# Kernel optimization log

Measured on AMD Instinct MI355X. Metric: run time of the kernel, lower is better.

The kernel has to match this reference:

```python
import jax, jax.numpy as jnp
import numpy as np

B, N, D, H = 128, 256, 256, 256
N_POWER_ITERS = 5  # matches spectral_norm(n_power_iterations=5)


def setup_inputs() -> dict:
    key = jax.random.key(0)
    ks = jax.random.split(key, 8)
    w = lambda k, shape: jax.random.normal(k, shape, dtype=jnp.float32) * 0.05
    return {
        "x": jax.random.normal(ks[0], (B, N, D), dtype=jnp.float32),
        "Wq": w(ks[1], (H, D)), "bq": w(ks[2], (H,)),
        "Wk": w(ks[3], (H, D)), "bk": w(ks[4], (H,)),
        "Wv": w(ks[5], (D, D)), "bv": w(ks[6], (D,)),
        "u0": jax.random.normal(ks[7], (D,), dtype=jnp.float32),
    }


def _l2norm(v, eps=1e-12):
    return v / (jnp.linalg.norm(v) + eps)


def _spectral_normalize(W, u0):
    # torch spectral_norm: power iteration (no grad) to get u, v; sigma = u^T W v (with grad)
    u = _l2norm(u0)
    v = _l2norm(W.T @ u)
    def body(i, uv):
        u, v = uv
        v = _l2norm(W.T @ u)
        u = _l2norm(W @ v)
        return (u, v)
    u, v = jax.lax.fori_loop(0, N_POWER_ITERS, body, (u, v))
    u = jax.lax.stop_gradient(u)
    v = jax.lax.stop_gradient(v)
    sigma = u @ (W @ v)
    return W / sigma


def reference(x, Wq, bq, Wk, bk, Wv, bv, u0):
    # torch Linear: y = x @ W.T + b, W is [out, in]
    q = jnp.einsum('bnd,hd->bnh', x, Wq) + bq          # [B, N, H]
    k = jnp.einsum('bnd,hd->bnh', x, Wk) + bk          # [B, N, H]
    Wv_sn = _spectral_normalize(Wv, u0)
    vals = jnp.einsum('bnd,od->bno', x, Wv_sn) + bv    # [B, N, D]
    scores = jnp.einsum('bnh,bmh->bnm', q, k)          # [B, N, N]
    # track_grads=False -> eigenvals detached; stop_gradient input so eig has no tangent path
    ev = jnp.linalg.eigvals(jax.lax.stop_gradient(scores))  # complex [B, N]
    rho = jnp.max(jnp.abs(ev), axis=-1)[:, None, None]      # spectral radius [B,1,1]
    attention = scores / rho
    weighted = jnp.einsum('bnm,bmd->bnd', attention, vals)  # [B, N, D]
    return weighted, attention
```

## Files before the change

kernel.cpp:

```cpp
#include <hip/hip_runtime.h>
#include <hip/hip_bf16.h>


#define NB 128
#define MAT 65536
#define BIG 8388608LL

typedef __attribute__((ext_vector_type(4))) float floatx4;
typedef __attribute__((ext_vector_type(4))) float f4v;
typedef __attribute__((ext_vector_type(8))) short short8v;
typedef __attribute__((ext_vector_type(4))) short short4v;

__device__ __forceinline__ short f2bf(float x) {
  union { float f; unsigned u; } v; v.f = x;
  unsigned r = v.u + 0x7fff + ((v.u >> 16) & 1);
  return (short)(r >> 16);
}
__device__ __forceinline__ float bf2f(short h) {
  union { unsigned u; float f; } v; v.u = ((unsigned)(unsigned short)h) << 16; return v.f;
}

template<bool TB, bool BATCHED>
__global__ __launch_bounds__(256) void gemm_mfma(
    const float* __restrict__ A, const float* __restrict__ B, float* __restrict__ C,
    long long sA, long long sB, long long sC,
    const float* __restrict__ bias,
    const float* __restrict__ scale_ptr, int sstride, int smode,
    float* __restrict__ norm_out,
    float* __restrict__ att_out,
    const float* __restrict__ B2, const float* __restrict__ bias2, float* __restrict__ C2,
    const float* __restrict__ B3, float* __restrict__ C3,
    const float* __restrict__ bsc, const float* __restrict__ bsb)
{
  __shared__ short sAhi[128 * 32], sAlo[128 * 32];
  __shared__ short sBhi[128 * 40], sBlo[128 * 40];

  int bz, m0, n0;
  if constexpr (BATCHED) {
    int lin = blockIdx.x;
    int xcd = lin & 7;
    int s = lin >> 3;
    bz = xcd * 16 + (s >> 2);
    int tile = s & 3;
    m0 = (tile >> 1) * 128;
    n0 = (tile & 1) * 128;
  } else {
    bz = 0;
    m0 = blockIdx.y * 128;
    n0 = (blockIdx.x & 1) * 128;
    int sel = blockIdx.x >> 1;
    if (sel == 1) { B = B2; bias = bias2; C = C2; }
    else if (sel == 2) { B = B3; bias = nullptr; C = C3; }
  }
  A += (long long)bz * sA;
  B += (long long)bz * sB;
  C += (long long)bz * sC;

  const int t = threadIdx.x;
  const int lane = t & 63;
  const int wave = t >> 6;
  const int wm = wave >> 1, wn = wave & 1;
  const int q = lane >> 4, c16 = lane & 15;

  float alpha = 1.0f;
  if (smode == 1) alpha = 1.0f / scale_ptr[bz * sstride];
  else if (smode == 2) alpha = scale_ptr[bz * sstride];
  else if (smode == 3) {
    float a2 = 0.f, w = 1.0f;
    #pragma unroll
    for (int i2 = 0; i2 <= 12; i2++) {
      const float* p = scale_ptr + i2 * 512 + bz * 4;
      a2 += w * 0.5f * logf(p[0] + p[1] + p[2] + p[3]);
      w *= 0.5f;
    }
    alpha = expf(-a2);
  }

  float rinv_att = alpha;
  const bool do_att = (att_out != nullptr) && (n0 == 0);

  float binv = 1.0f;
  if (bsc) binv = 1.0f / bsc[0];

  floatx4 acc[4][4];
  #pragma unroll
  for (int i = 0; i < 4; i++)
    #pragma unroll
    for (int j = 0; j < 4; j++)
      acc[i][j] = (floatx4){0.f, 0.f, 0.f, 0.f};

  for (int k0 = 0; k0 < 256; k0 += 32) {
    #pragma unroll
    for (int i = 0; i < 4; i++) {
      int f = t + i * 256;
      int row = f >> 3, c4 = f & 7;
      f4v v = *(const f4v*)(A + (long long)(m0 + row) * 256 + k0 + c4 * 4);
      if (do_att)
        *(f4v*)(att_out + (long long)bz * MAT + (long long)(m0 + row) * 256 + k0 + c4 * 4)
            = v * rinv_att;
      short4v h, l;
      #pragma unroll
      for (int e = 0; e < 4; e++) {
        short hh = f2bf(v[e]);
        h[e] = hh;
        l[e] = f2bf(v[e] - bf2f(hh));
      }
      *(short4v*)&sAhi[row * 32 + c4 * 4] = h;
      *(short4v*)&sAlo[row * 32 + c4 * 4] = l;
    }
    if constexpr (TB) {
      #pragma unroll
      for (int i = 0; i < 4; i++) {
        int f = t + i * 256;
        int row = f >> 3, c4 = f & 7;
        f4v v = *(const f4v*)(B + (long long)(n0 + row) * 256 + k0 + c4 * 4);
        short4v h, l;
        #pragma unroll
        for (int e = 0; e < 4; e++) {
          short hh = f2bf(v[e]);
          h[e] = hh;
          l[e] = f2bf(v[e] - bf2f(hh));
        }
        *(short4v*)&sBhi[row * 40 + c4 * 4] = h;
        *(short4v*)&sBlo[row * 40 + c4 * 4] = l;
      }
      __syncthreads();
    } else {
      __shared__ float sT[32 * 132];
      #pragma unroll
      for (int i = 0; i < 4; i++) {
        int f = t + i * 256;
        int kk = f >> 5, n4 = f & 31;
        f4v v = *(const f4v*)(B + (long long)(k0 + kk) * 256 + n0 + n4 * 4);
        if (bsb) {
          #pragma unroll
          for (int e = 0; e < 4; e++) v[e] = v[e] * binv + bsb[n0 + n4 * 4 + e];
        }
        *(f4v*)&sT[kk * 132 + n4 * 4] = v;
      }
      __syncthreads();
      int n = t & 127, kh = t >> 7;
      short8v h0, h1, l0, l1;
      #pragma unroll
      for (int j = 0; j < 8; j++) {
        float x0 = sT[(kh * 16 + j) * 132 + n];
        float x1 = sT[(kh * 16 + 8 + j) * 132 + n];
        short a0 = f2bf(x0), a1 = f2bf(x1);
        h0[j] = a0; l0[j] = f2bf(x0 - bf2f(a0));
        h1[j] = a1; l1[j] = f2bf(x1 - bf2f(a1));
      }
      *(short8v*)&sBhi[n * 40 + kh * 16] = h0;
      *(short8v*)&sBhi[n * 40 + kh * 16 + 8] = h1;
      *(short8v*)&sBlo[n * 40 + kh * 16] = l0;
      *(short8v*)&sBlo[n * 40 + kh * 16 + 8] = l1;
      __syncthreads();
    }

    short8v ah[4], al[4], bh[4], bl[4];
    #pragma unroll
    for (int fi = 0; fi < 4; fi++) {
      int r = wm * 64 + fi * 16 + c16;
      ah[fi] = *(short8v*)&sAhi[r * 32 + q * 8];
      al[fi] = *(short8v*)&sAlo[r * 32 + q * 8];
    }
    #pragma unroll
    for (int fj = 0; fj < 4; fj++) {
      int r = wn * 64 + fj * 16 + c16;
      bh[fj] = *(short8v*)&sBhi[r * 40 + q * 8];
      bl[fj] = *(short8v*)&sBlo[r * 40 + q * 8];
    }
    #pragma unroll
    for (int fi = 0; fi < 4; fi++)
      #pragma unroll
      for (int fj = 0; fj < 4; fj++) {
        acc[fi][fj] = __builtin_amdgcn_mfma_f32_16x16x32_bf16(al[fi], bh[fj], acc[fi][fj], 0, 0, 0);
        acc[fi][fj] = __builtin_amdgcn_mfma_f32_16x16x32_bf16(ah[fi], bl[fj], acc[fi][fj], 0, 0, 0);
        acc[fi][fj] = __builtin_amdgcn_mfma_f32_16x16x32_bf16(ah[fi], bh[fj], acc[fi][fj], 0, 0, 0);
      }
    __syncthreads();
  }

  float ssq = 0.f;
  #pragma unroll
  for (int fi = 0; fi < 4; fi++) {
    #pragma unroll
    for (int fj = 0; fj < 4; fj++) {
      int col = n0 + wn * 64 + fj * 16 + c16;
      float bb = bias ? bias[col] : 0.f;
      #pragma unroll
      for (int r = 0; r < 4; r++) {
        int row = m0 + wm * 64 + fi * 16 + q * 4 + r;
        float v = acc[fi][fj][r] * alpha + bb;
        C[(long long)row * 256 + col] = v;
        ssq += v * v;
      }
    }
  }

  if (norm_out) {
    float* red = (float*)sAhi;
    red[t] = ssq;
    __syncthreads();
    for (int off = 128; off > 0; off >>= 1) {
      if (t < off) red[t] += red[t + off];
      __syncthreads();
    }
    if (t == 0) {
      int tl = ((m0 >> 7) << 1) | (n0 >> 7);
      norm_out[bz * 4 + tl] = red[0];
    }
  }
}

__device__ __forceinline__ void chain_epilogue(
    short* LB, float* red, floatx4 (&acc)[4][4], float alpha,
    int m0, int n0, int wm, int wn, int q, int c16, int t,
    short* __restrict__ Mout,
    float* __restrict__ nout, int bz, int tile, bool write_out)
{
  __syncthreads();
  float ssq = 0.f;
  #pragma unroll
  for (int fi = 0; fi < 4; fi++)
    #pragma unroll
    for (int fj = 0; fj < 4; fj++) {
      int lcol = wn * 64 + fj * 16 + c16;
      #pragma unroll
      for (int r = 0; r < 4; r++) {
        int lrow = wm * 64 + fi * 16 + q * 4 + r;
        float v = acc[fi][fj][r] * alpha;
        ssq += v * v;
        if (write_out) LB[lrow * 128 + lcol] = f2bf(v);
      }
    }

  if (write_out) {
    __syncthreads();
    int lr = t >> 1, off = (t & 1) * 64;
    #pragma unroll
    for (int jc = 0; jc < 8; jc++)
      *(short8v*)(Mout + (long long)(m0 + lr) * 256 + n0 + off + jc * 8)
          = *(const short8v*)&LB[lr * 128 + off + jc * 8];
  }

  red[t] = ssq;
  __syncthreads();
  for (int off2 = 128; off2 > 0; off2 >>= 1) {
    if (t < off2) red[t] += red[t + off2];
    __syncthreads();
  }
  if (t == 0) nout[bz * 4 + tile] = red[0];
}

__global__ __launch_bounds__(256) void sq_f32bf(
    const float* __restrict__ S, short* __restrict__ Mo,
    const float* __restrict__ nprev, float* __restrict__ nout)
{
  __shared__ short SM[18432];
  __shared__ float sT[32 * 132];
  __shared__ float red[256];
  short* sAhi = SM;
  short* sAlo = SM + 4096;
  short* sBhi = SM + 8192;
  short* sBlo = SM + 13312;

  int lin = blockIdx.x;
  int xcd = lin & 7, s = lin >> 3;
  int bz = xcd * 16 + (s >> 2);
  int tile = s & 3;
  int m0 = (tile >> 1) * 128, n0 = (tile & 1) * 128;
  const float* A = S + (long long)bz * MAT;

  const int t = threadIdx.x;
  const int lane = t & 63;
  const int wave = t >> 6;
  const int wm = wave >> 1, wn = wave & 1;
  const int q = lane >> 4, c16 = lane & 15;

  floatx4 acc[4][4];
  #pragma unroll
  for (int i = 0; i < 4; i++)
    #pragma unroll
    for (int j = 0; j < 4; j++)
      acc[i][j] = (floatx4){0.f, 0.f, 0.f, 0.f};

  for (int k0 = 0; k0 < 256; k0 += 32) {
    #pragma unroll
    for (int i = 0; i < 4; i++) {
      int f = t + i * 256;
      int row = f >> 3, c4 = f & 7;
      f4v v = *(const f4v*)(A + (long long)(m0 + row) * 256 + k0 + c4 * 4);
      short4v h, l;
      #pragma unroll
      for (int e = 0; e < 4; e++) {
        short hh = f2bf(v[e]);
        h[e] = hh;
        l[e] = f2bf(v[e] - bf2f(hh));
      }
      *(short4v*)&sAhi[row * 32 + c4 * 4] = h;
      *(short4v*)&sAlo[row * 32 + c4 * 4] = l;
    }
    #pragma unroll
    for (int i = 0; i < 4; i++) {
      int f = t + i * 256;
      int kk = f >> 5, n4 = f & 31;
      f4v v = *(const f4v*)(A + (long long)(k0 + kk) * 256 + n0 + n4 * 4);
      *(f4v*)&sT[kk * 132 + n4 * 4] = v;
    }
    __syncthreads();
    {
      int n = t & 127, kh = t >> 7;
      short8v h0, h1, l0, l1;
      #pragma unroll
      for (int j = 0; j < 8; j++) {
        float x0 = sT[(kh * 16 + j) * 132 + n];
        float x1 = sT[(kh * 16 + 8 + j) * 132 + n];
        short a0 = f2bf(x0), a1 = f2bf(x1);
        h0[j] = a0; l0[j] = f2bf(x0 - bf2f(a0));
        h1[j] = a1; l1[j] = f2bf(x1 - bf2f(a1));
      }
      *(short8v*)&sBhi[n * 40 + kh * 16] = h0;
      *(short8v*)&sBhi[n * 40 + kh * 16 + 8] = h1;
      *(short8v*)&sBlo[n * 40 + kh * 16] = l0;
      *(short8v*)&sBlo[n * 40 + kh * 16 + 8] = l1;
    }
    __syncthreads();

    short8v ah[4], al[4], bh[4], bl[4];
    #pragma unroll
    for (int fi = 0; fi < 4; fi++) {
      int r = wm * 64 + fi * 16 + c16;
      ah[fi] = *(short8v*)&sAhi[r * 32 + q * 8];
      al[fi] = *(short8v*)&sAlo[r * 32 + q * 8];
    }
    #pragma unroll
    for (int fj = 0; fj < 4; fj++) {
      int r = wn * 64 + fj * 16 + c16;
      bh[fj] = *(short8v*)&sBhi[r * 40 + q * 8];
      bl[fj] = *(short8v*)&sBlo[r * 40 + q * 8];
    }
    #pragma unroll
    for (int fi = 0; fi < 4; fi++)
      #pragma unroll
      for (int fj = 0; fj < 4; fj++) {
        acc[fi][fj] = __builtin_amdgcn_mfma_f32_16x16x32_bf16(al[fi], bh[fj], acc[fi][fj], 0, 0, 0);
        acc[fi][fj] = __builtin_amdgcn_mfma_f32_16x16x32_bf16(ah[fi], bl[fj], acc[fi][fj], 0, 0, 0);
        acc[fi][fj] = __builtin_amdgcn_mfma_f32_16x16x32_bf16(ah[fi], bh[fj], acc[fi][fj], 0, 0, 0);
      }
    __syncthreads();
  }

  const float* p = nprev + bz * 4;
  float alpha = 1.0f / (p[0] + p[1] + p[2] + p[3]);
  chain_epilogue(SM, red, acc, alpha, m0, n0, wm, wn, q, c16, t,
                 Mo + (long long)bz * MAT, nout, bz, tile, true);
}

template<bool WRITE_OUT>
__global__ __launch_bounds__(256) void sq_bf(
    const short* __restrict__ Mi, short* __restrict__ Mo,
    const float* __restrict__ nprev, float* __restrict__ nout)
{
  __shared__ short SMEM[16384];
  __shared__ float red[256];
  short* Bs = SMEM;

  int lin = blockIdx.x;
  int xcd = lin & 7, s = lin >> 3;
  int bz = xcd * 16 + (s >> 2);
  int tile = s & 3;
  int m0 = (tile >> 1) * 128, n0 = (tile & 1) * 128;

  const short* A = Mi + (long long)bz * MAT;

  const int t = threadIdx.x;
  const int lane = t & 63;
  const int wave = t >> 6;
  const int wm = wave >> 1, wn = wave & 1;
  const int q = lane >> 4, c16 = lane & 15;
  const int g = t >> 5, cc = t & 31;

  floatx4 acc[4][4];
  #pragma unroll
  for (int i = 0; i < 4; i++)
    #pragma unroll
    for (int j = 0; j < 4; j++)
      acc[i][j] = (floatx4){0.f, 0.f, 0.f, 0.f};

  for (int k0 = 0; k0 < 256; k0 += 32) {
    __syncthreads();
    short4v r0 = *(const short4v*)(A + (long long)(k0 + g * 4 + 0) * 256 + n0 + cc * 4);
    short4v r1 = *(const short4v*)(A + (long long)(k0 + g * 4 + 1) * 256 + n0 + cc * 4);
    short4v r2 = *(const short4v*)(A + (long long)(k0 + g * 4 + 2) * 256 + n0 + cc * 4);
    short4v r3 = *(const short4v*)(A + (long long)(k0 + g * 4 + 3) * 256 + n0 + cc * 4);
    #pragma unroll
    for (int j = 0; j < 4; j++) {
      short4v w4 = (short4v){r0[j], r1[j], r2[j], r3[j]};
      *(short4v*)&Bs[(cc * 4 + j) * 36 + g * 4] = w4;
    }
    __syncthreads();

    short8v a[4], b[4];
    #pragma unroll
    for (int fi = 0; fi < 4; fi++)
      a[fi] = *(const short8v*)(A + (long long)(m0 + wm * 64 + fi * 16 + c16) * 256 + k0 + q * 8);
    #pragma unroll
    for (int fj = 0; fj < 4; fj++) {
      int n = wn * 64 + fj * 16 + c16;
      short4v lo = *(const short4v*)&Bs[n * 36 + q * 8];
      short4v hi = *(const short4v*)&Bs[n * 36 + q * 8 + 4];
      b[fj] = __builtin_shufflevector(lo, hi, 0, 1, 2, 3, 4, 5, 6, 7);
    }
    #pragma unroll
    for (int fi = 0; fi < 4; fi++)
      #pragma unroll
      for (int fj = 0; fj < 4; fj++)
        acc[fi][fj] = __builtin_amdgcn_mfma_f32_16x16x32_bf16(a[fi], b[fj], acc[fi][fj], 0, 0, 0);
  }

  const float* p = nprev + bz * 4;
  float alpha = 1.0f / (p[0] + p[1] + p[2] + p[3]);
  chain_epilogue(SMEM, red, acc, alpha, m0, n0, wm, wn, q, c16, t,
                 WRITE_OUT ? Mo + (long long)bz * MAT : nullptr,
                 nout, bz, tile, WRITE_OUT);
}

__device__ __forceinline__ float bsum1024(float x, float* red, int t)
{
  red[t] = x; __syncthreads();
  for (int off = 512; off > 0; off >>= 1) {
    if (t < off) red[t] += red[t + off];
    __syncthreads();
  }
  float r = red[0];
  __syncthreads();
  return r;
}

__global__ __launch_bounds__(1024) void sigma_kernel(
    const float* __restrict__ W, const float* __restrict__ u0, float* __restrict__ sigma)
{
  __shared__ short Wl[65536];
  __shared__ float u[256], v[256], red[1024];
  int t = threadIdx.x;
  int r = t & 255, seg = t >> 8;
  const float eps = 1e-12f;

  #pragma unroll
  for (int i = 0; i < 16; i++) {
    int idx = (i * 1024 + t) * 4;
    f4v w = *(const f4v*)(W + idx);
    short4v h;
    #pragma unroll
    for (int e = 0; e < 4; e++) h[e] = f2bf(w[e]);
    *(short4v*)&Wl[idx] = h;
  }

  float x = (t < 256) ? u0[t] : 0.f;
  float nrm = sqrtf(bsum1024(x * x, red, t));
  if (t < 256) u[t] = x / (nrm + eps);
  __syncthreads();

  for (int it = 0; it < 5; it++) {
    float sv = 0.f;
    #pragma unroll 8
    for (int j = 0; j < 64; j++) {
      int h = seg * 64 + j;
      sv = fmaf(bf2f(Wl[h * 256 + r]), u[h], sv);
    }
    red[t] = sv; __syncthreads();
    float vr = 0.f;
    if (t < 256) vr = red[t] + red[256 + t] + red[512 + t] + red[768 + t];
    __syncthreads();
    nrm = sqrtf(bsum1024(t < 256 ? vr * vr : 0.f, red, t));
    if (t < 256) v[t] = vr / (nrm + eps);
    __syncthreads();
    if (it < 4) {
      float su = 0.f;
      #pragma unroll
      for (int j = 0; j < 16; j++) {
        short4v w4 = *(const short4v*)&Wl[r * 256 + seg * 64 + j * 4];
        const float* vv = &v[seg * 64 + j * 4];
        su += bf2f(w4[0]) * vv[0] + bf2f(w4[1]) * vv[1]
            + bf2f(w4[2]) * vv[2] + bf2f(w4[3]) * vv[3];
      }
      red[t] = su; __syncthreads();
      float ur = 0.f;
      if (t < 256) ur = red[t] + red[256 + t] + red[512 + t] + red[768 + t];
      __syncthreads();
      nrm = sqrtf(bsum1024(t < 256 ? ur * ur : 0.f, red, t));
      if (t < 256) u[t] = ur / (nrm + eps);
      __syncthreads();
    }
  }

  float z = 0.f;
  #pragma unroll
  for (int j = 0; j < 16; j++) {
    f4v w = *(const f4v*)(W + r * 256 + seg * 64 + j * 4);
    const float* vv = &v[seg * 64 + j * 4];
    z += w[0] * vv[0] + w[1] * vv[1] + w[2] * vv[2] + w[3] * vv[3];
  }
  red[t] = z; __syncthreads();
  float zr = 0.f;
  if (t < 256) zr = red[t] + red[256 + t] + red[512 + t] + red[768 + t];
  __syncthreads();
  float zz = bsum1024(t < 256 ? zr * zr : 0.f, red, t);
  if (t == 0) sigma[0] = sqrtf(zz);
}

extern "C" void kernel_launch(void* const* d_in, const int* in_sizes, int n_in,
                              void* d_out, int out_size, void* d_ws, size_t ws_size,
                              hipStream_t stream)
{
  const float* x  = (const float*)d_in[0];
  const float* Wq = (const float*)d_in[1];
  const float* bq = (const float*)d_in[2];
  const float* Wk = (const float*)d_in[3];
  const float* bk = (const float*)d_in[4];
  const float* Wv = (const float*)d_in[5];
  const float* bv = (const float*)d_in[6];
  const float* u0 = (const float*)d_in[7];

  float* out  = (float*)d_out;
  float* out0 = out;
  float* out1 = out + BIG;
  short* out0s = (short*)out0;
  short* out1s = (short*)out1;

  float* ws         = (float*)d_ws;
  float* scores_buf = ws;
  float* vals_buf   = ws + BIG;
  float* partials   = ws + 2 * BIG;
  float* sigma      = partials + 13 * 512;

  dim3 blk(256);

  gemm_mfma<true, false><<<dim3(6, 256, 1), blk, 0, stream>>>(
      x, Wq, out0, 0, 0, 0, bq, nullptr, 0, 0, nullptr, nullptr,
      Wk, bk, out1, Wv, vals_buf, nullptr, nullptr);

  gemm_mfma<true, true><<<dim3(512, 1, 1), blk, 0, stream>>>(
      out0, out1, scores_buf, MAT, MAT, MAT, nullptr, nullptr, 0, 0, partials,
      nullptr, nullptr, nullptr, nullptr, nullptr, nullptr, nullptr, nullptr);

  sigma_kernel<<<1, dim3(1024), 0, stream>>>(Wv, u0, sigma);

  sq_f32bf<<<dim3(512, 1, 1), blk, 0, stream>>>(scores_buf, out0s, partials, partials + 512);

  const short* cin = out0s;
  for (int i = 0; i < 10; i++) {
    short* cout = (i & 1) ? out0s : out1s;
    sq_bf<true><<<dim3(512, 1, 1), blk, 0, stream>>>(cin, cout,
        partials + (1 + i) * 512, partials + (2 + i) * 512);
    cin = cout;
  }
  sq_bf<false><<<dim3(512, 1, 1), blk, 0, stream>>>(cin, nullptr,
      partials + 11 * 512, partials + 12 * 512);

  gemm_mfma<false, true><<<dim3(512, 1, 1), blk, 0, stream>>>(
      scores_buf, vals_buf, out0, MAT, MAT, MAT, nullptr, partials, 0, 3, nullptr,
      out1, nullptr, nullptr, nullptr, nullptr, nullptr, sigma, bv);
}
```

Measured before the change: 503.7 us.

## Fuse repeated matrix-squaring chain into one LDS-resident kernel per batch

Replaces the eleven separate bf16 matrix-squaring launches with a single kernel per batch that keeps the whole 256x256 bf16 matrix in LDS with an XOR swizzle. All squaring steps, the Frobenius norms and the log-weighted spectral-radius estimate are computed inside that kernel, and only a per-batch inverse rho goes to the final GEMM. This removes per-step global round-trips and launch overhead. In exchange it uses only 128 blocks of 1024 threads with about 144KB of LDS each, which limits occupancy and parallelism, and it computes rho in-kernel instead of in the final GEMM epilogue.

```diff
diff --git a/kernel.cpp b/kernel.cpp
--- a/kernel.cpp
+++ b/kernel.cpp
@@ -356,73 +356,110 @@
                  Mo + (long long)bz * MAT, nout, bz, tile, true);
 }
 
-template<bool WRITE_OUT>
-__global__ __launch_bounds__(256) void sq_bf(
-    const short* __restrict__ Mi, short* __restrict__ Mo,
-    const float* __restrict__ nprev, float* __restrict__ nout)
-{
-  __shared__ short SMEM[16384];
-  __shared__ float red[256];
-  short* Bs = SMEM;
-
-  int lin = blockIdx.x;
-  int xcd = lin & 7, s = lin >> 3;
-  int bz = xcd * 16 + (s >> 2);
-  int tile = s & 3;
-  int m0 = (tile >> 1) * 128, n0 = (tile & 1) * 128;
-
-  const short* A = Mi + (long long)bz * MAT;
-
+__device__ __forceinline__ int midx(int row, int col) {
+  return row * 256 + (col ^ ((row & 7) << 3));
+}
+
+__global__ __launch_bounds__(1024, 4) void chain_fused(
+    const short* __restrict__ M1, const float* __restrict__ partials,
+    float* __restrict__ rho_inv)
+{
+  __shared__ short M[65536];
+  __shared__ short Bs[8192];
+  __shared__ float red[16];
+
+  const int bz = blockIdx.x;
   const int t = threadIdx.x;
   const int lane = t & 63;
   const int wave = t >> 6;
-  const int wm = wave >> 1, wn = wave & 1;
+  const int wm = wave >> 2, wn = wave & 3;
   const int q = lane >> 4, c16 = lane & 15;
-  const int g = t >> 5, cc = t & 31;
-
-  floatx4 acc[4][4];
-  #pragma unroll
-  for (int i = 0; i < 4; i++)
-    #pragma unroll
-    for (int j = 0; j < 4; j++)
-      acc[i][j] = (floatx4){0.f, 0.f, 0.f, 0.f};
-
-  for (int k0 = 0; k0 < 256; k0 += 32) {
-    __syncthreads();
-    short4v r0 = *(const short4v*)(A + (long long)(k0 + g * 4 + 0) * 256 + n0 + cc * 4);
-    short4v r1 = *(const short4v*)(A + (long long)(k0 + g * 4 + 1) * 256 + n0 + cc * 4);
-    short4v r2 = *(const short4v*)(A + (long long)(k0 + g * 4 + 2) * 256 + n0 + cc * 4);
-    short4v r3 = *(const short4v*)(A + (long long)(k0 + g * 4 + 3) * 256 + n0 + cc * 4);
-    #pragma unroll
-    for (int j = 0; j < 4; j++) {
-      short4v w4 = (short4v){r0[j], r1[j], r2[j], r3[j]};
-      *(short4v*)&Bs[(cc * 4 + j) * 36 + g * 4] = w4;
-    }
-    __syncthreads();
-
-    short8v a[4], b[4];
+  const int sn = t & 255;
+  const int skh = t >> 8;
+
+  const short* src = M1 + (long long)bz * MAT;
+  #pragma unroll
+  for (int i = 0; i < 8; i++) {
+    int chunk = t + i * 1024;
+    int row = chunk >> 5, col8 = (chunk & 31) * 8;
+    short8v v = *(const short8v*)(src + chunk * 8);
+    *(short8v*)&M[midx(row, col8)] = v;
+  }
+
+  const float* p0 = partials + bz * 4;
+  const float* p1 = partials + 512 + bz * 4;
+  float n0 = p0[0] + p0[1] + p0[2] + p0[3];
+  float nprev = p1[0] + p1[1] + p1[2] + p1[3];
+  float a2 = 0.5f * logf(n0) + 0.25f * logf(nprev);
+  float w = 0.25f;
+
+  __syncthreads();
+
+  #pragma unroll 1
+  for (int s = 2; s <= 12; s++) {
+    float alpha = 1.0f / nprev;
+    floatx4 acc[4][4];
+    #pragma unroll
+    for (int i = 0; i < 4; i++)
+      #pragma unroll
+      for (int j = 0; j < 4; j++)
+        acc[i][j] = (floatx4){0.f, 0.f, 0.f, 0.f};
+
+    for (int k0 = 0; k0 < 256; k0 += 32) {
+      if (k0) __syncthreads();
+      short8v sv;
+      #pragma unroll
+      for (int j = 0; j < 8; j++)
+        sv[j] = M[midx(k0 + skh * 8 + j, sn)];
+      *(short8v*)&Bs[sn * 32 + ((skh ^ (sn & 3)) << 3)] = sv;
+      __syncthreads();
+
+      short8v b[4];
+      #pragma unroll
+      for (int fj = 0; fj < 4; fj++) {
+        int n = wn * 64 + fj * 16 + c16;
+        b[fj] = *(const short8v*)&Bs[n * 32 + ((q ^ (n & 3)) << 3)];
+      }
+      #pragma unroll
+      for (int fi = 0; fi < 4; fi++) {
+        int r = wm * 64 + fi * 16 + c16;
+        short8v a = *(const short8v*)&M[midx(r, k0 + q * 8)];
+        #pragma unroll
+        for (int fj = 0; fj < 4; fj++)
+          acc[fi][fj] = __builtin_amdgcn_mfma_f32_16x16x32_bf16(a, b[fj], acc[fi][fj], 0, 0, 0);
+      }
+    }
+    __syncthreads();
+
+    float ssq = 0.f;
     #pragma unroll
     for (int fi = 0; fi < 4; fi++)
-      a[fi] = *(const short8v*)(A + (long long)(m0 + wm * 64 + fi * 16 + c16) * 256 + k0 + q * 8);
-    #pragma unroll
-    for (int fj = 0; fj < 4; fj++) {
-      int n = wn * 64 + fj * 16 + c16;
-      short4v lo = *(const short4v*)&Bs[n * 36 + q * 8];
-      short4v hi = *(const short4v*)&Bs[n * 36 + q * 8 + 4];
-      b[fj] = __builtin_shufflevector(lo, hi, 0, 1, 2, 3, 4, 5, 6, 7);
-    }
-    #pragma unroll
-    for (int fi = 0; fi < 4; fi++)
-      #pragma unroll
-      for (int fj = 0; fj < 4; fj++)
-        acc[fi][fj] = __builtin_amdgcn_mfma_f32_16x16x32_bf16(a[fi], b[fj], acc[fi][fj], 0, 0, 0);
-  }
-
-  const float* p = nprev + bz * 4;
-  float alpha = 1.0f / (p[0] + p[1] + p[2] + p[3]);
-  chain_epilogue(SMEM, red, acc, alpha, m0, n0, wm, wn, q, c16, t,
-                 WRITE_OUT ? Mo + (long long)bz * MAT : nullptr,
-                 nout, bz, tile, WRITE_OUT);
+      #pragma unroll
+      for (int fj = 0; fj < 4; fj++) {
+        int col = wn * 64 + fj * 16 + c16;
+        #pragma unroll
+        for (int r = 0; r < 4; r++) {
+          int row = wm * 64 + fi * 16 + q * 4 + r;
+          float v = acc[fi][fj][r] * alpha;
+          ssq += v * v;
+          if (s < 12) M[midx(row, col)] = f2bf(v);
+        }
+      }
+
+    #pragma unroll
+    for (int off = 32; off > 0; off >>= 1)
+      ssq += __shfl_xor(ssq, off, 64);
+    if (lane == 0) red[wave] = ssq;
+    __syncthreads();
+    float tot = 0.f;
+    #pragma unroll
+    for (int i = 0; i < 16; i++) tot += red[i];
+    w *= 0.5f;
+    a2 += w * logf(tot);
+    nprev = tot;
+  }
+
+  if (t == 0) rho_inv[bz] = expf(-a2);
 }
 
 __device__ __forceinline__ float bsum1024(float x, float* red, int t)
@@ -526,13 +563,13 @@
   float* out0 = out;
   float* out1 = out + BIG;
   short* out0s = (short*)out0;
-  short* out1s = (short*)out1;
 
   float* ws         = (float*)d_ws;
   float* scores_buf = ws;
   float* vals_buf   = ws + BIG;
   float* partials   = ws + 2 * BIG;
   float* sigma      = partials + 13 * 512;
+  float* rho_inv    = partials + 1024;
 
   dim3 blk(256);
 
@@ -548,17 +585,9 @@
 
   sq_f32bf<<<dim3(512, 1, 1), blk, 0, stream>>>(scores_buf, out0s, partials, partials + 512);
 
-  const short* cin = out0s;
-  for (int i = 0; i < 10; i++) {
-    short* cout = (i & 1) ? out0s : out1s;
-    sq_bf<true><<<dim3(512, 1, 1), blk, 0, stream>>>(cin, cout,
-        partials + (1 + i) * 512, partials + (2 + i) * 512);
-    cin = cout;
-  }
-  sq_bf<false><<<dim3(512, 1, 1), blk, 0, stream>>>(cin, nullptr,
-      partials + 11 * 512, partials + 12 * 512);
+  chain_fused<<<dim3(128, 1, 1), dim3(1024, 1, 1), 0, stream>>>(out0s, partials, rho_inv);
 
   gemm_mfma<false, true><<<dim3(512, 1, 1), blk, 0, stream>>>(
-      scores_buf, vals_buf, out0, MAT, MAT, MAT, nullptr, partials, 0, 3, nullptr,
+      scores_buf, vals_buf, out0, MAT, MAT, MAT, nullptr, rho_inv, 1, 2, nullptr,
       out1, nullptr, nullptr, nullptr, nullptr, nullptr, sigma, bv);
 }
```

After: 635.7 us. +26.2%, slower.

## Fuse repeated-squaring chain into one persistent kernel with per-batch barriers

Applied to the files above, without the earlier changes.

Replaces the sq_f32bf launch plus eleven sq_bf launches with a single persistent kernel, chain_l2. Its 512 blocks synchronize per batch through atomic counters in global memory instead of kernel boundaries. The kernel also accumulates the log-norm weighted sum on device and writes rho_inv directly, so the final GEMM reads a precomputed scale. This removes launch gaps and tail effects across the 12 chained steps, at the cost of spin-wait barriers and an added memset. It depends on all 512 blocks being co-resident (launch bounds 256,2), otherwise it can deadlock.

```diff
diff --git a/kernel.cpp b/kernel.cpp
--- a/kernel.cpp
+++ b/kernel.cpp
@@ -252,24 +252,34 @@
   if (t == 0) nout[bz * 4 + tile] = red[0];
 }
 
-__global__ __launch_bounds__(256) void sq_f32bf(
-    const float* __restrict__ S, short* __restrict__ Mo,
-    const float* __restrict__ nprev, float* __restrict__ nout)
+__device__ __forceinline__ void batch_bar(int* __restrict__ bar, int idx, int t)
+{
+  __syncthreads();
+  if (t == 0) {
+    __threadfence();
+    atomicAdd(bar + idx, 1);
+    while (__hip_atomic_load(bar + idx, __ATOMIC_RELAXED, __HIP_MEMORY_SCOPE_AGENT) < 4)
+      __builtin_amdgcn_s_sleep(1);
+    __threadfence();
+  }
+  __syncthreads();
+}
+
+__global__ __launch_bounds__(256, 2) void chain_l2(
+    const float* __restrict__ S,
+    short* __restrict__ Ma, short* __restrict__ Mb,
+    float* __restrict__ partials, int* __restrict__ bar,
+    float* __restrict__ rho_inv)
 {
   __shared__ short SM[18432];
   __shared__ float sT[32 * 132];
   __shared__ float red[256];
-  short* sAhi = SM;
-  short* sAlo = SM + 4096;
-  short* sBhi = SM + 8192;
-  short* sBlo = SM + 13312;
-
-  int lin = blockIdx.x;
-  int xcd = lin & 7, s = lin >> 3;
-  int bz = xcd * 16 + (s >> 2);
-  int tile = s & 3;
-  int m0 = (tile >> 1) * 128, n0 = (tile & 1) * 128;
-  const float* A = S + (long long)bz * MAT;
+
+  const int lin = blockIdx.x;
+  const int xcd = lin & 7, sI = lin >> 3;
+  const int bz = xcd * 16 + (sI >> 2);
+  const int tile = sI & 3;
+  const int m0 = (tile >> 1) * 128, n0 = (tile & 1) * 128;
 
   const int t = threadIdx.x;
   const int lane = t & 63;
@@ -277,152 +287,165 @@
   const int wm = wave >> 1, wn = wave & 1;
   const int q = lane >> 4, c16 = lane & 15;
 
-  floatx4 acc[4][4];
-  #pragma unroll
-  for (int i = 0; i < 4; i++)
-    #pragma unroll
-    for (int j = 0; j < 4; j++)
-      acc[i][j] = (floatx4){0.f, 0.f, 0.f, 0.f};
-
-  for (int k0 = 0; k0 < 256; k0 += 32) {
-    #pragma unroll
-    for (int i = 0; i < 4; i++) {
-      int f = t + i * 256;
-      int row = f >> 3, c4 = f & 7;
-      f4v v = *(const f4v*)(A + (long long)(m0 + row) * 256 + k0 + c4 * 4);
-      short4v h, l;
-      #pragma unroll
-      for (int e = 0; e < 4; e++) {
-        short hh = f2bf(v[e]);
-        h[e] = hh;
-        l[e] = f2bf(v[e] - bf2f(hh));
-      }
-      *(short4v*)&sAhi[row * 32 + c4 * 4] = h;
-      *(short4v*)&sAlo[row * 32 + c4 * 4] = l;
-    }
-    #pragma unroll
-    for (int i = 0; i < 4; i++) {
-      int f = t + i * 256;
-      int kk = f >> 5, n4 = f & 31;
-      f4v v = *(const f4v*)(A + (long long)(k0 + kk) * 256 + n0 + n4 * 4);
-      *(f4v*)&sT[kk * 132 + n4 * 4] = v;
-    }
-    __syncthreads();
-    {
-      int n = t & 127, kh = t >> 7;
-      short8v h0, h1, l0, l1;
-      #pragma unroll
-      for (int j = 0; j < 8; j++) {
-        float x0 = sT[(kh * 16 + j) * 132 + n];
-        float x1 = sT[(kh * 16 + 8 + j) * 132 + n];
-        short a0 = f2bf(x0), a1 = f2bf(x1);
-        h0[j] = a0; l0[j] = f2bf(x0 - bf2f(a0));
-        h1[j] = a1; l1[j] = f2bf(x1 - bf2f(a1));
-      }
-      *(short8v*)&sBhi[n * 40 + kh * 16] = h0;
-      *(short8v*)&sBhi[n * 40 + kh * 16 + 8] = h1;
-      *(short8v*)&sBlo[n * 40 + kh * 16] = l0;
-      *(short8v*)&sBlo[n * 40 + kh * 16 + 8] = l1;
-    }
-    __syncthreads();
-
-    short8v ah[4], al[4], bh[4], bl[4];
-    #pragma unroll
-    for (int fi = 0; fi < 4; fi++) {
-      int r = wm * 64 + fi * 16 + c16;
-      ah[fi] = *(short8v*)&sAhi[r * 32 + q * 8];
-      al[fi] = *(short8v*)&sAlo[r * 32 + q * 8];
-    }
-    #pragma unroll
-    for (int fj = 0; fj < 4; fj++) {
-      int r = wn * 64 + fj * 16 + c16;
-      bh[fj] = *(short8v*)&sBhi[r * 40 + q * 8];
-      bl[fj] = *(short8v*)&sBlo[r * 40 + q * 8];
-    }
-    #pragma unroll
-    for (int fi = 0; fi < 4; fi++)
+  const float* pp = partials + bz * 4;
+  float nprev = pp[0] + pp[1] + pp[2] + pp[3];
+  float a2 = 0.5f * logf(nprev);
+  float w = 0.5f;
+
+  {
+    short* sAhi = SM;
+    short* sAlo = SM + 4096;
+    short* sBhi = SM + 8192;
+    short* sBlo = SM + 13312;
+    const float* A = S + (long long)bz * MAT;
+    const float alpha = 1.0f / nprev;
+
+    floatx4 acc[4][4];
+    #pragma unroll
+    for (int i = 0; i < 4; i++)
+      #pragma unroll
+      for (int j = 0; j < 4; j++)
+        acc[i][j] = (floatx4){0.f, 0.f, 0.f, 0.f};
+
+    for (int k0 = 0; k0 < 256; k0 += 32) {
+      #pragma unroll
+      for (int i = 0; i < 4; i++) {
+        int f = t + i * 256;
+        int row = f >> 3, c4 = f & 7;
+        f4v v = *(const f4v*)(A + (long long)(m0 + row) * 256 + k0 + c4 * 4);
+        short4v h, l;
+        #pragma unroll
+        for (int e = 0; e < 4; e++) {
+          short hh = f2bf(v[e]);
+          h[e] = hh;
+          l[e] = f2bf(v[e] - bf2f(hh));
+        }
+        *(short4v*)&sAhi[row * 32 + c4 * 4] = h;
+        *(short4v*)&sAlo[row * 32 + c4 * 4] = l;
+      }
+      #pragma unroll
+      for (int i = 0; i < 4; i++) {
+        int f = t + i * 256;
+        int kk = f >> 5, n4 = f & 31;
+        f4v v = *(const f4v*)(A + (long long)(k0 + kk) * 256 + n0 + n4 * 4);
+        *(f4v*)&sT[kk * 132 + n4 * 4] = v;
+      }
+      __syncthreads();
+      {
+        int n = t & 127, kh = t >> 7;
+        short8v h0, h1, l0, l1;
+        #pragma unroll
+        for (int j = 0; j < 8; j++) {
+          float x0 = sT[(kh * 16 + j) * 132 + n];
+          float x1 = sT[(kh * 16 + 8 + j) * 132 + n];
+          short a0 = f2bf(x0), a1 = f2bf(x1);
+          h0[j] = a0; l0[j] = f2bf(x0 - bf2f(a0));
+          h1[j] = a1; l1[j] = f2bf(x1 - bf2f(a1));
+        }
+        *(short8v*)&sBhi[n * 40 + kh * 16] = h0;
+        *(short8v*)&sBhi[n * 40 + kh * 16 + 8] = h1;
+        *(short8v*)&sBlo[n * 40 + kh * 16] = l0;
+        *(short8v*)&sBlo[n * 40 + kh * 16 + 8] = l1;
+      }
+      __syncthreads();
+
+      short8v ah[4], al[4], bh[4], bl[4];
+      #pragma unroll
+      for (int fi = 0; fi < 4; fi++) {
+        int r = wm * 64 + fi * 16 + c16;
+        ah[fi] = *(short8v*)&sAhi[r * 32 + q * 8];
+        al[fi] = *(short8v*)&sAlo[r * 32 + q * 8];
+      }
       #pragma unroll
       for (int fj = 0; fj < 4; fj++) {
-        acc[fi][fj] = __builtin_amdgcn_mfma_f32_16x16x32_bf16(al[fi], bh[fj], acc[fi][fj], 0, 0, 0);
-        acc[fi][fj] = __builtin_amdgcn_mfma_f32_16x16x32_bf16(ah[fi], bl[fj], acc[fi][fj], 0, 0, 0);
-        acc[fi][fj] = __builtin_amdgcn_mfma_f32_16x16x32_bf16(ah[fi], bh[fj], acc[fi][fj], 0, 0, 0);
-      }
-    __syncthreads();
-  }
-
-  const float* p = nprev + bz * 4;
-  float alpha = 1.0f / (p[0] + p[1] + p[2] + p[3]);
-  chain_epilogue(SM, red, acc, alpha, m0, n0, wm, wn, q, c16, t,
-                 Mo + (long long)bz * MAT, nout, bz, tile, true);
-}
-
-template<bool WRITE_OUT>
-__global__ __launch_bounds__(256) void sq_bf(
-    const short* __restrict__ Mi, short* __restrict__ Mo,
-    const float* __restrict__ nprev, float* __restrict__ nout)
-{
-  __shared__ short SMEM[16384];
-  __shared__ float red[256];
-  short* Bs = SMEM;
-
-  int lin = blockIdx.x;
-  int xcd = lin & 7, s = lin >> 3;
-  int bz = xcd * 16 + (s >> 2);
-  int tile = s & 3;
-  int m0 = (tile >> 1) * 128, n0 = (tile & 1) * 128;
-
-  const short* A = Mi + (long long)bz * MAT;
-
-  const int t = threadIdx.x;
-  const int lane = t & 63;
-  const int wave = t >> 6;
-  const int wm = wave >> 1, wn = wave & 1;
-  const int q = lane >> 4, c16 = lane & 15;
+        int r = wn * 64 + fj * 16 + c16;
+        bh[fj] = *(short8v*)&sBhi[r * 40 + q * 8];
+        bl[fj] = *(short8v*)&sBlo[r * 40 + q * 8];
+      }
+      #pragma unroll
+      for (int fi = 0; fi < 4; fi++)
+        #pragma unroll
+        for (int fj = 0; fj < 4; fj++) {
+          acc[fi][fj] = __builtin_amdgcn_mfma_f32_16x16x32_bf16(al[fi], bh[fj], acc[fi][fj], 0, 0, 0);
+          acc[fi][fj] = __builtin_amdgcn_mfma_f32_16x16x32_bf16(ah[fi], bl[fj], acc[fi][fj], 0, 0, 0);
+          acc[fi][fj] = __builtin_amdgcn_mfma_f32_16x16x32_bf16(ah[fi], bh[fj], acc[fi][fj], 0, 0, 0);
+        }
+      __syncthreads();
+    }
+
+    chain_epilogue(SM, red, acc, alpha, m0, n0, wm, wn, q, c16, t,
+                   Ma + (long long)bz * MAT, partials + 512, bz, tile, true);
+  }
+  batch_bar(bar, 0 * NB + bz, t);
+  {
+    const float* p = partials + 512 + bz * 4;
+    nprev = p[0] + p[1] + p[2] + p[3];
+    w *= 0.5f;
+    a2 += w * logf(nprev);
+  }
+
+  const short* cin = Ma;
+  short* cout = Mb;
   const int g = t >> 5, cc = t & 31;
 
-  floatx4 acc[4][4];
-  #pragma unroll
-  for (int i = 0; i < 4; i++)
-    #pragma unroll
-    for (int j = 0; j < 4; j++)
-      acc[i][j] = (floatx4){0.f, 0.f, 0.f, 0.f};
-
-  for (int k0 = 0; k0 < 256; k0 += 32) {
-    __syncthreads();
-    short4v r0 = *(const short4v*)(A + (long long)(k0 + g * 4 + 0) * 256 + n0 + cc * 4);
-    short4v r1 = *(const short4v*)(A + (long long)(k0 + g * 4 + 1) * 256 + n0 + cc * 4);
-    short4v r2 = *(const short4v*)(A + (long long)(k0 + g * 4 + 2) * 256 + n0 + cc * 4);
-    short4v r3 = *(const short4v*)(A + (long long)(k0 + g * 4 + 3) * 256 + n0 + cc * 4);
-    #pragma unroll
-    for (int j = 0; j < 4; j++) {
-      short4v w4 = (short4v){r0[j], r1[j], r2[j], r3[j]};
-      *(short4v*)&Bs[(cc * 4 + j) * 36 + g * 4] = w4;
-    }
-    __syncthreads();
-
-    short8v a[4], b[4];
-    #pragma unroll
-    for (int fi = 0; fi < 4; fi++)
-      a[fi] = *(const short8v*)(A + (long long)(m0 + wm * 64 + fi * 16 + c16) * 256 + k0 + q * 8);
-    #pragma unroll
-    for (int fj = 0; fj < 4; fj++) {
-      int n = wn * 64 + fj * 16 + c16;
-      short4v lo = *(const short4v*)&Bs[n * 36 + q * 8];
-      short4v hi = *(const short4v*)&Bs[n * 36 + q * 8 + 4];
-      b[fj] = __builtin_shufflevector(lo, hi, 0, 1, 2, 3, 4, 5, 6, 7);
-    }
-    #pragma unroll
-    for (int fi = 0; fi < 4; fi++)
-      #pragma unroll
-      for (int fj = 0; fj < 4; fj++)
-        acc[fi][fj] = __builtin_amdgcn_mfma_f32_16x16x32_bf16(a[fi], b[fj], acc[fi][fj], 0, 0, 0);
-  }
-
-  const float* p = nprev + bz * 4;
-  float alpha = 1.0f / (p[0] + p[1] + p[2] + p[3]);
-  chain_epilogue(SMEM, red, acc, alpha, m0, n0, wm, wn, q, c16, t,
-                 WRITE_OUT ? Mo + (long long)bz * MAT : nullptr,
-                 nout, bz, tile, WRITE_OUT);
+  #pragma unroll 1
+  for (int s = 2; s <= 12; s++) {
+    const float alpha = 1.0f / nprev;
+    const short* A = cin + (long long)bz * MAT;
+    short* Bs = SM;
+
+    floatx4 acc[4][4];
+    #pragma unroll
+    for (int i = 0; i < 4; i++)
+      #pragma unroll
+      for (int j = 0; j < 4; j++)
+        acc[i][j] = (floatx4){0.f, 0.f, 0.f, 0.f};
+
+    for (int k0 = 0; k0 < 256; k0 += 32) {
+      __syncthreads();
+      short4v r0 = *(const short4v*)(A + (long long)(k0 + g * 4 + 0) * 256 + n0 + cc * 4);
+      short4v r1 = *(const short4v*)(A + (long long)(k0 + g * 4 + 1) * 256 + n0 + cc * 4);
+      short4v r2 = *(const short4v*)(A + (long long)(k0 + g * 4 + 2) * 256 + n0 + cc * 4);
+      short4v r3 = *(const short4v*)(A + (long long)(k0 + g * 4 + 3) * 256 + n0 + cc * 4);
+      #pragma unroll
+      for (int j = 0; j < 4; j++) {
+        short4v w4 = (short4v){r0[j], r1[j], r2[j], r3[j]};
+        *(short4v*)&Bs[(cc * 4 + j) * 36 + g * 4] = w4;
+      }
+      __syncthreads();
+
+      short8v a[4], b[4];
+      #pragma unroll
+      for (int fi = 0; fi < 4; fi++)
+        a[fi] = *(const short8v*)(A + (long long)(m0 + wm * 64 + fi * 16 + c16) * 256 + k0 + q * 8);
+      #pragma unroll
+      for (int fj = 0; fj < 4; fj++) {
+        int n = wn * 64 + fj * 16 + c16;
+        short4v lo = *(const short4v*)&Bs[n * 36 + q * 8];
+        short4v hi = *(const short4v*)&Bs[n * 36 + q * 8 + 4];
+        b[fj] = __builtin_shufflevector(lo, hi, 0, 1, 2, 3, 4, 5, 6, 7);
+      }
+      #pragma unroll
+      for (int fi = 0; fi < 4; fi++)
+        #pragma unroll
+        for (int fj = 0; fj < 4; fj++)
+          acc[fi][fj] = __builtin_amdgcn_mfma_f32_16x16x32_bf16(a[fi], b[fj], acc[fi][fj], 0, 0, 0);
+    }
+
+    const bool wr = (s < 12);
+    chain_epilogue(SM, red, acc, alpha, m0, n0, wm, wn, q, c16, t,
+                   wr ? cout + (long long)bz * MAT : nullptr,
+                   partials + s * 512, bz, tile, wr);
+    batch_bar(bar, (s - 1) * NB + bz, t);
+    const float* p = partials + s * 512 + bz * 4;
+    nprev = p[0] + p[1] + p[2] + p[3];
+    w *= 0.5f;
+    a2 += w * logf(nprev);
+
+    const short* tmp = cin; cin = cout; cout = (short*)tmp;
+  }
+
+  if (tile == 0 && t == 0) rho_inv[bz] = expf(-a2);
 }
 
 __device__ __forceinline__ float bsum1024(float x, float* red, int t)
@@ -533,8 +556,12 @@
   float* vals_buf   = ws + BIG;
   float* partials   = ws + 2 * BIG;
   float* sigma      = partials + 13 * 512;
+  float* rho_inv    = sigma + 4;
+  int*   bar        = (int*)(rho_inv + 128);
 
   dim3 blk(256);
+
+  hipMemsetAsync(bar, 0, 12 * NB * sizeof(int), stream);
 
   gemm_mfma<true, false><<<dim3(6, 256, 1), blk, 0, stream>>>(
       x, Wq, out0, 0, 0, 0, bq, nullptr, 0, 0, nullptr, nullptr,
@@ -546,19 +573,10 @@
 
   sigma_kernel<<<1, dim3(1024), 0, stream>>>(Wv, u0, sigma);
 
-  sq_f32bf<<<dim3(512, 1, 1), blk, 0, stream>>>(scores_buf, out0s, partials, partials + 512);
-
-  const short* cin = out0s;
-  for (int i = 0; i < 10; i++) {
-    short* cout = (i & 1) ? out0s : out1s;
-    sq_bf<true><<<dim3(512, 1, 1), blk, 0, stream>>>(cin, cout,
-        partials + (1 + i) * 512, partials + (2 + i) * 512);
-    cin = cout;
-  }
-  sq_bf<false><<<dim3(512, 1, 1), blk, 0, stream>>>(cin, nullptr,
-      partials + 11 * 512, partials + 12 * 512);
+  chain_l2<<<dim3(512, 1, 1), blk, 0, stream>>>(
+      scores_buf, out0s, out1s, partials, bar, rho_inv);
 
   gemm_mfma<false, true><<<dim3(512, 1, 1), blk, 0, stream>>>(
-      scores_buf, vals_buf, out0, MAT, MAT, MAT, nullptr, partials, 0, 3, nullptr,
+      scores_buf, vals_buf, out0, MAT, MAT, MAT, nullptr, rho_inv, 1, 2, nullptr,
       out1, nullptr, nullptr, nullptr, nullptr, nullptr, sigma, bv);
 }
```

New measurement: 985.8 us. 1.96x slower.

## Pre-split weights to bf16 hi/lo and store q/k as split bf16

Applied to the files above, without the earlier changes.

Adds a kernel that splits Wq/Wk/Wv once into bf16 hi/lo pairs. A new fused projection kernel computes q and k together, sharing the split x tile, and writes q/k directly as hi/lo bf16 planes. The scores GEMM then loads these pre-split operands straight from global memory without any LDS staging or per-tile conversion. The per-block log/exp spectral-radius computation moves into a tiny finalize kernel that the last GEMM reads as a plain scale. This adds two small launches, and the scores kernel now depends on uncached direct global loads.

```diff
diff --git a/kernel.cpp b/kernel.cpp
--- a/kernel.cpp
+++ b/kernel.cpp
@@ -65,16 +65,6 @@
   float alpha = 1.0f;
   if (smode == 1) alpha = 1.0f / scale_ptr[bz * sstride];
   else if (smode == 2) alpha = scale_ptr[bz * sstride];
-  else if (smode == 3) {
-    float a2 = 0.f, w = 1.0f;
-    #pragma unroll
-    for (int i2 = 0; i2 <= 12; i2++) {
-      const float* p = scale_ptr + i2 * 512 + bz * 4;
-      a2 += w * 0.5f * logf(p[0] + p[1] + p[2] + p[3]);
-      w *= 0.5f;
-    }
-    alpha = expf(-a2);
-  }
 
   float rinv_att = alpha;
   const bool do_att = (att_out != nullptr) && (n0 == 0);
@@ -212,6 +202,277 @@
   }
 }
 
+__global__ __launch_bounds__(256) void split_w(
+    const float* __restrict__ Wq, const float* __restrict__ Wk,
+    const float* __restrict__ Wv, short* __restrict__ ws6)
+{
+  int gid = blockIdx.x * 256 + threadIdx.x;
+  int m = gid >> 14;
+  int off = (gid & 16383) * 4;
+  const float* src = (m == 0) ? Wq : (m == 1) ? Wk : Wv;
+  f4v v = *(const f4v*)(src + off);
+  short4v h, l;
+  #pragma unroll
+  for (int e = 0; e < 4; e++) {
+    short hh = f2bf(v[e]);
+    h[e] = hh;
+    l[e] = f2bf(v[e] - bf2f(hh));
+  }
+  *(short4v*)&ws6[(long long)(m * 2) * MAT + off] = h;
+  *(short4v*)&ws6[(long long)(m * 2 + 1) * MAT + off] = l;
+}
+
+__global__ __launch_bounds__(256, 2) void proj3(
+    const float* __restrict__ x, const short* __restrict__ wsp,
+    const float* __restrict__ bq, const float* __restrict__ bk,
+    short* __restrict__ qhi, short* __restrict__ qlo,
+    short* __restrict__ khi, short* __restrict__ klo,
+    float* __restrict__ vals)
+{
+  __shared__ short sAhi[128 * 40], sAlo[128 * 40];
+
+  const int n0 = (blockIdx.x & 1) * 128;
+  const int grp = blockIdx.x >> 1;
+  const int m0 = blockIdx.y * 128;
+
+  const int t = threadIdx.x;
+  const int lane = t & 63;
+  const int wave = t >> 6;
+  const int wm = wave >> 1, wn = wave & 1;
+  const int q = lane >> 4, c16 = lane & 15;
+
+  if (grp == 0) {
+    floatx4 acc0[4][4], acc1[4][4];
+    #pragma unroll
+    for (int i = 0; i < 4; i++)
+      #pragma unroll
+      for (int j = 0; j < 4; j++) {
+        acc0[i][j] = (floatx4){0.f, 0.f, 0.f, 0.f};
+        acc1[i][j] = (floatx4){0.f, 0.f, 0.f, 0.f};
+      }
+
+    for (int k0 = 0; k0 < 256; k0 += 32) {
+      if (k0) __syncthreads();
+      #pragma unroll
+      for (int i = 0; i < 4; i++) {
+        int f = t + i * 256;
+        int row = f >> 3, c4 = f & 7;
+        f4v v = *(const f4v*)(x + (long long)(m0 + row) * 256 + k0 + c4 * 4);
+        short4v h, l;
+        #pragma unroll
+        for (int e = 0; e < 4; e++) {
+          short hh = f2bf(v[e]);
+          h[e] = hh;
+          l[e] = f2bf(v[e] - bf2f(hh));
+        }
+        *(short4v*)&sAhi[row * 40 + c4 * 4] = h;
+        *(short4v*)&sAlo[row * 40 + c4 * 4] = l;
+      }
+      __syncthreads();
+
+      short8v ah[4], al[4];
+      #pragma unroll
+      for (int fi = 0; fi < 4; fi++) {
+        int r = wm * 64 + fi * 16 + c16;
+        ah[fi] = *(short8v*)&sAhi[r * 40 + q * 8];
+        al[fi] = *(short8v*)&sAlo[r * 40 + q * 8];
+      }
+      {
+        short8v bh[4], bl[4];
+        #pragma unroll
+        for (int fj = 0; fj < 4; fj++) {
+          long long r = (long long)(n0 + wn * 64 + fj * 16 + c16) * 256 + k0 + q * 8;
+          bh[fj] = *(const short8v*)(wsp + r);
+          bl[fj] = *(const short8v*)(wsp + MAT + r);
+        }
+        #pragma unroll
+        for (int fi = 0; fi < 4; fi++)
+          #pragma unroll
+          for (int fj = 0; fj < 4; fj++) {
+            acc0[fi][fj] = __builtin_amdgcn_mfma_f32_16x16x32_bf16(al[fi], bh[fj], acc0[fi][fj], 0, 0, 0);
+            acc0[fi][fj] = __builtin_amdgcn_mfma_f32_16x16x32_bf16(ah[fi], bl[fj], acc0[fi][fj], 0, 0, 0);
+            acc0[fi][fj] = __builtin_amdgcn_mfma_f32_16x16x32_bf16(ah[fi], bh[fj], acc0[fi][fj], 0, 0, 0);
+          }
+      }
+      {
+        short8v bh[4], bl[4];
+        #pragma unroll
+        for (int fj = 0; fj < 4; fj++) {
+          long long r = (long long)(n0 + wn * 64 + fj * 16 + c16) * 256 + k0 + q * 8;
+          bh[fj] = *(const short8v*)(wsp + 2LL * MAT + r);
+          bl[fj] = *(const short8v*)(wsp + 3LL * MAT + r);
+        }
+        #pragma unroll
+        for (int fi = 0; fi < 4; fi++)
+          #pragma unroll
+          for (int fj = 0; fj < 4; fj++) {
+            acc1[fi][fj] = __builtin_amdgcn_mfma_f32_16x16x32_bf16(al[fi], bh[fj], acc1[fi][fj], 0, 0, 0);
+            acc1[fi][fj] = __builtin_amdgcn_mfma_f32_16x16x32_bf16(ah[fi], bl[fj], acc1[fi][fj], 0, 0, 0);
+            acc1[fi][fj] = __builtin_amdgcn_mfma_f32_16x16x32_bf16(ah[fi], bh[fj], acc1[fi][fj], 0, 0, 0);
+          }
+      }
+    }
+
+    #pragma unroll
+    for (int fi = 0; fi < 4; fi++)
+      #pragma unroll
+      for (int fj = 0; fj < 4; fj++) {
+        int col = n0 + wn * 64 + fj * 16 + c16;
+        float bbq = bq[col], bbk = bk[col];
+        #pragma unroll
+        for (int r = 0; r < 4; r++) {
+          long long row = m0 + wm * 64 + fi * 16 + q * 4 + r;
+          float vq = acc0[fi][fj][r] + bbq;
+          float vk = acc1[fi][fj][r] + bbk;
+          short hq = f2bf(vq), hk = f2bf(vk);
+          qhi[row * 256 + col] = hq;
+          qlo[row * 256 + col] = f2bf(vq - bf2f(hq));
+          khi[row * 256 + col] = hk;
+          klo[row * 256 + col] = f2bf(vk - bf2f(hk));
+        }
+      }
+  } else {
+    floatx4 acc[4][4];
+    #pragma unroll
+    for (int i = 0; i < 4; i++)
+      #pragma unroll
+      for (int j = 0; j < 4; j++)
+        acc[i][j] = (floatx4){0.f, 0.f, 0.f, 0.f};
+
+    for (int k0 = 0; k0 < 256; k0 += 32) {
+      if (k0) __syncthreads();
+      #pragma unroll
+      for (int i = 0; i < 4; i++) {
+        int f = t + i * 256;
+        int row = f >> 3, c4 = f & 7;
+        f4v v = *(const f4v*)(x + (long long)(m0 + row) * 256 + k0 + c4 * 4);
+        short4v h, l;
+        #pragma unroll
+        for (int e = 0; e < 4; e++) {
+          short hh = f2bf(v[e]);
+          h[e] = hh;
+          l[e] = f2bf(v[e] - bf2f(hh));
+        }
+        *(short4v*)&sAhi[row * 40 + c4 * 4] = h;
+        *(short4v*)&sAlo[row * 40 + c4 * 4] = l;
+      }
+      __syncthreads();
+
+      short8v ah[4], al[4], bh[4], bl[4];
+      #pragma unroll
+      for (int fi = 0; fi < 4; fi++) {
+        int r = wm * 64 + fi * 16 + c16;
+        ah[fi] = *(short8v*)&sAhi[r * 40 + q * 8];
+        al[fi] = *(short8v*)&sAlo[r * 40 + q * 8];
+      }
+      #pragma unroll
+      for (int fj = 0; fj < 4; fj++) {
+        long long r = (long long)(n0 + wn * 64 + fj * 16 + c16) * 256 + k0 + q * 8;
+        bh[fj] = *(const short8v*)(wsp + 4LL * MAT + r);
+        bl[fj] = *(const short8v*)(wsp + 5LL * MAT + r);
+      }
+      #pragma unroll
+      for (int fi = 0; fi < 4; fi++)
+        #pragma unroll
+        for (int fj = 0; fj < 4; fj++) {
+          acc[fi][fj] = __builtin_amdgcn_mfma_f32_16x16x32_bf16(al[fi], bh[fj], acc[fi][fj], 0, 0, 0);
+          acc[fi][fj] = __builtin_amdgcn_mfma_f32_16x16x32_bf16(ah[fi], bl[fj], acc[fi][fj], 0, 0, 0);
+          acc[fi][fj] = __builtin_amdgcn_mfma_f32_16x16x32_bf16(ah[fi], bh[fj], acc[fi][fj], 0, 0, 0);
+        }
+    }
+
+    #pragma unroll
+    for (int fi = 0; fi < 4; fi++)
+      #pragma unroll
+      for (int fj = 0; fj < 4; fj++) {
+        int col = n0 + wn * 64 + fj * 16 + c16;
+        #pragma unroll
+        for (int r = 0; r < 4; r++) {
+          long long row = m0 + wm * 64 + fi * 16 + q * 4 + r;
+          vals[row * 256 + col] = acc[fi][fj][r];
+        }
+      }
+  }
+}
+
+__global__ __launch_bounds__(256) void scores_direct(
+    const short* __restrict__ qhi, const short* __restrict__ qlo,
+    const short* __restrict__ khi, const short* __restrict__ klo,
+    float* __restrict__ S, float* __restrict__ norm_out)
+{
+  __shared__ float red[256];
+
+  const int lin = blockIdx.x;
+  const int xcd = lin & 7, s = lin >> 3;
+  const int bz = xcd * 16 + (s >> 2);
+  const int tile = s & 3;
+  const int m0 = (tile >> 1) * 128, n0 = (tile & 1) * 128;
+
+  const int t = threadIdx.x;
+  const int lane = t & 63;
+  const int wave = t >> 6;
+  const int wm = wave >> 1, wn = wave & 1;
+  const int q = lane >> 4, c16 = lane & 15;
+
+  floatx4 acc[4][4];
+  #pragma unroll
+  for (int i = 0; i < 4; i++)
+    #pragma unroll
+    for (int j = 0; j < 4; j++)
+      acc[i][j] = (floatx4){0.f, 0.f, 0.f, 0.f};
+
+  const long long arow = (long long)(bz * 256 + m0 + wm * 64) * 256;
+  const long long brow = (long long)(bz * 256 + n0 + wn * 64) * 256;
+
+  for (int k0 = 0; k0 < 256; k0 += 32) {
+    short8v ah[4], al[4], bh[4], bl[4];
+    #pragma unroll
+    for (int fi = 0; fi < 4; fi++) {
+      long long r = arow + (long long)(fi * 16 + c16) * 256 + k0 + q * 8;
+      ah[fi] = *(const short8v*)(qhi + r);
+      al[fi] = *(const short8v*)(qlo + r);
+    }
+    #pragma unroll
+    for (int fj = 0; fj < 4; fj++) {
+      long long r = brow + (long long)(fj * 16 + c16) * 256 + k0 + q * 8;
+      bh[fj] = *(const short8v*)(khi + r);
+      bl[fj] = *(const short8v*)(klo + r);
+    }
+    #pragma unroll
+    for (int fi = 0; fi < 4; fi++)
+      #pragma unroll
+      for (int fj = 0; fj < 4; fj++) {
+        acc[fi][fj] = __builtin_amdgcn_mfma_f32_16x16x32_bf16(al[fi], bh[fj], acc[fi][fj], 0, 0, 0);
+        acc[fi][fj] = __builtin_amdgcn_mfma_f32_16x16x32_bf16(ah[fi], bl[fj], acc[fi][fj], 0, 0, 0);
+        acc[fi][fj] = __builtin_amdgcn_mfma_f32_16x16x32_bf16(ah[fi], bh[fj], acc[fi][fj], 0, 0, 0);
+      }
+  }
+
+  float* C = S + (long long)bz * MAT;
+  float ssq = 0.f;
+  #pragma unroll
+  for (int fi = 0; fi < 4; fi++)
+    #pragma unroll
+    for (int fj = 0; fj < 4; fj++) {
+      int col = n0 + wn * 64 + fj * 16 + c16;
+      #pragma unroll
+      for (int r = 0; r < 4; r++) {
+        int row = m0 + wm * 64 + fi * 16 + q * 4 + r;
+        float v = acc[fi][fj][r];
+        C[(long long)row * 256 + col] = v;
+        ssq += v * v;
+      }
+    }
+
+  red[t] = ssq;
+  __syncthreads();
+  for (int off = 128; off > 0; off >>= 1) {
+    if (t < off) red[t] += red[t + off];
+    __syncthreads();
+  }
+  if (t == 0) norm_out[bz * 4 + tile] = red[0];
+}
+
 __device__ __forceinline__ void chain_epilogue(
     short* LB, float* red, floatx4 (&acc)[4][4], float alpha,
     int m0, int n0, int wm, int wn, int q, int c16, int t,
@@ -423,6 +684,20 @@
   chain_epilogue(SMEM, red, acc, alpha, m0, n0, wm, wn, q, c16, t,
                  WRITE_OUT ? Mo + (long long)bz * MAT : nullptr,
                  nout, bz, tile, WRITE_OUT);
+}
+
+__global__ __launch_bounds__(128) void rho_finalize(
+    const float* __restrict__ partials, float* __restrict__ rho_inv)
+{
+  int bz = threadIdx.x;
+  float a2 = 0.f, w = 1.0f;
+  #pragma unroll
+  for (int i2 = 0; i2 <= 12; i2++) {
+    const float* p = partials + i2 * 512 + bz * 4;
+    a2 += w * 0.5f * logf(p[0] + p[1] + p[2] + p[3]);
+    w *= 0.5f;
+  }
+  rho_inv[bz] = expf(-a2);
 }
 
 __device__ __forceinline__ float bsum1024(float x, float* red, int t)
@@ -528,21 +803,28 @@
   short* out0s = (short*)out0;
   short* out1s = (short*)out1;
 
+  short* qhi = out0s;
+  short* qlo = out0s + 32768LL * 256;
+  short* khi = out1s;
+  short* klo = out1s + 32768LL * 256;
+
   float* ws         = (float*)d_ws;
   float* scores_buf = ws;
   float* vals_buf   = ws + BIG;
   float* partials   = ws + 2 * BIG;
   float* sigma      = partials + 13 * 512;
+  float* rho_inv    = sigma + 4;
+  short* wsplit     = (short*)ws;
 
   dim3 blk(256);
 
-  gemm_mfma<true, false><<<dim3(6, 256, 1), blk, 0, stream>>>(
-      x, Wq, out0, 0, 0, 0, bq, nullptr, 0, 0, nullptr, nullptr,
-      Wk, bk, out1, Wv, vals_buf, nullptr, nullptr);
-
-  gemm_mfma<true, true><<<dim3(512, 1, 1), blk, 0, stream>>>(
-      out0, out1, scores_buf, MAT, MAT, MAT, nullptr, nullptr, 0, 0, partials,
-      nullptr, nullptr, nullptr, nullptr, nullptr, nullptr, nullptr, nullptr);
+  split_w<<<dim3(192, 1, 1), blk, 0, stream>>>(Wq, Wk, Wv, wsplit);
+
+  proj3<<<dim3(4, 256, 1), blk, 0, stream>>>(
+      x, wsplit, bq, bk, qhi, qlo, khi, klo, vals_buf);
+
+  scores_direct<<<dim3(512, 1, 1), blk, 0, stream>>>(
+      qhi, qlo, khi, klo, scores_buf, partials);
 
   sigma_kernel<<<1, dim3(1024), 0, stream>>>(Wv, u0, sigma);
 
@@ -558,7 +840,9 @@
   sq_bf<false><<<dim3(512, 1, 1), blk, 0, stream>>>(cin, nullptr,
       partials + 11 * 512, partials + 12 * 512);
 
+  rho_finalize<<<1, dim3(128), 0, stream>>>(partials, rho_inv);
+
   gemm_mfma<false, true><<<dim3(512, 1, 1), blk, 0, stream>>>(
-      scores_buf, vals_buf, out0, MAT, MAT, MAT, nullptr, partials, 0, 3, nullptr,
+      scores_buf, vals_buf, out0, MAT, MAT, MAT, nullptr, rho_inv, 1, 2, nullptr,
       out1, nullptr, nullptr, nullptr, nullptr, nullptr, sigma, bv);
 }
```

New measurement: 529.6 us. 1.05x slower.
